# Kernel tuning notes

Hardware: AMD Instinct MI355X
Metric: run time of the kernel (lower is better)

## Reference

```python
import jax, jax.numpy as jnp
import numpy as np

N, E, D_IN, L, H, U = 20000, 320000, 256, 4, 4, 64
HID = H * U  # 256
OUT = 64
LN_EPS = 1e-3  # keras LayerNormalization default epsilon
NEG_SLOPE = 0.2


def layer_norm(x, g, b):
    m = jnp.mean(x, axis=-1, keepdims=True)
    v = jnp.var(x, axis=-1, keepdims=True)
    return (x - m) * jax.lax.rsqrt(v + LN_EPS) * g + b


def gatv2(x, dst, src, Wl, Wr, a):
    # x: [N, HID]; Wl/Wr: [HID, H, U]; a: [H, U]
    zl = jnp.einsum('nd,dhu->nhu', x, Wl)  # target projection
    zr = jnp.einsum('nd,dhu->nhu', x, Wr)  # source projection / messages
    f = jax.nn.leaky_relu(zl[dst] + zr[src], NEG_SLOPE)       # [E, H, U]
    s = jnp.einsum('ehu,hu->eh', f, a)                        # [E, H]
    smax = jax.ops.segment_max(s, dst, num_segments=N)        # [N, H]
    es = jnp.exp(s - smax[dst])
    denom = jax.ops.segment_sum(es, dst, num_segments=N)      # [N, H]
    agg = jax.ops.segment_sum(es[:, :, None] * zr[src], dst, num_segments=N)
    agg = agg / (denom[:, :, None] + 1e-9)                    # [N, H, U]
    return agg.reshape(N, HID) + x  # residual (input dim == H*U)


def setup_inputs() -> dict:
    key = jax.random.key(0)
    ks = jax.random.split(key, 10)
    s_in = 1.0 / np.sqrt(D_IN)
    s_h = 1.0 / np.sqrt(HID)
    return {
        'x': jax.random.normal(ks[0], (N, D_IN), jnp.float32),
        'head_W': jax.random.normal(ks[1], (D_IN, HID), jnp.float32) * s_in,
        'head_b': jnp.zeros((HID,), jnp.float32),
        'ng_g': jnp.ones((L, HID), jnp.float32),
        'ng_b': jnp.zeros((L, HID), jnp.float32),
        'Wl': jax.random.normal(ks[2], (L, HID, H, U), jnp.float32) * s_h,
        'Wr': jax.random.normal(ks[3], (L, HID, H, U), jnp.float32) * s_h,
        'att': jax.random.normal(ks[4], (L, H, U), jnp.float32) * (1.0 / np.sqrt(U)),
        'nd_g': jnp.ones((L, HID), jnp.float32),
        'nd_b': jnp.zeros((L, HID), jnp.float32),
        'dense_W': jax.random.normal(ks[5], (L, HID, 4 * HID), jnp.float32) * s_h,
        'dense_b': jnp.zeros((L, 4 * HID), jnp.float32),
        'tail_W': jax.random.normal(ks[6], (HID, OUT), jnp.float32) * s_h,
        'tail_b': jnp.zeros((OUT,), jnp.float32),
        'edges': jax.random.randint(ks[7], (E, 2), 0, N, jnp.int32),
    }


def reference(x, head_W, head_b, ng_g, ng_b, Wl, Wr, att, nd_g, nd_b,
              dense_W, dense_b, tail_W, tail_b, edges):
    dst, src = edges[:, 0], edges[:, 1]
    h = x @ head_W + head_b  # head_layer
    for l in range(L):
        h = layer_norm(h, ng_g[l], ng_b[l])
        h = gatv2(h, dst, src, Wl[l], Wr[l], att[l])
        xr = layer_norm(h, nd_g[l], nd_b[l])
        # inference: dropout is identity
        d = jax.nn.gelu(xr @ dense_W[l] + dense_b[l], approximate=True)  # [N, 4*HID]
        h = d.reshape(N, 4, HID).sum(axis=1) + xr  # Add(split(.,4)) + residual
    return h @ tail_W + tail_b
```

## Files before the change

### kernel.cpp

```cpp
#include <hip/hip_runtime.h>
#include <cstdint>

#define NN 20000
#define EE 320000
#define DHID 256

typedef short bf16x8 __attribute__((ext_vector_type(8)));
typedef float f32x4 __attribute__((ext_vector_type(4)));


__device__ __forceinline__ float b2f(unsigned short u) {
    union { unsigned int i; float f; } v;
    v.i = ((unsigned int)u) << 16;
    return v.f;
}

__device__ __forceinline__ void b2f2(unsigned int w, float& lo, float& hi) {
    union { unsigned int i; float f; } a, c;
    a.i = w << 16;
    c.i = w & 0xffff0000u;
    lo = a.f;
    hi = c.f;
}

__device__ __forceinline__ unsigned short f2b(float x) {
    union { float f; unsigned int i; } v;
    v.f = x;
    unsigned int r = (v.i + 0x7FFFu + ((v.i >> 16) & 1u)) >> 16;
    return (unsigned short)r;
}

__device__ __forceinline__ float wave_sum(float v) {
#pragma unroll
    for (int m = 1; m < 64; m <<= 1) v += __shfl_xor(v, m);
    return v;
}

#define DPP_ROR_ADD(v, n)                                                                  \
    v += __int_as_float(__builtin_amdgcn_update_dpp(__float_as_int(v), __float_as_int(v),  \
                                                    0x120 + (n), 0xF, 0xF, 0))
__device__ __forceinline__ float quad16_sum(float v) {
    DPP_ROR_ADD(v, 8);
    DPP_ROR_ADD(v, 4);
    DPP_ROR_ADD(v, 2);
    DPP_ROR_ADD(v, 1);
    return v;
}

__device__ __forceinline__ float gelu_f(float x) {
    float z = 0.7978845608028654f * (x + 0.044715f * x * x * x);
    float e = __expf(2.0f * z);
    float t = 1.0f - 2.0f / (e + 1.0f);
    return 0.5f * x * (1.0f + t);
}

__device__ __forceinline__ void gld16(const unsigned short* g, unsigned short* lds) {
    __builtin_amdgcn_global_load_lds((const __attribute__((address_space(1))) unsigned int*)g,
                                     (__attribute__((address_space(3))) unsigned int*)lds, 16, 0, 0);
}


__global__ void hist_kernel(const int* __restrict__ edges, int* __restrict__ counts, int E_) {
    int e = blockIdx.x * 256 + threadIdx.x;
    if (e >= E_) return;
    atomicAdd(&counts[edges[e * 2]], 1);
}

__global__ void pad_counts(const int* __restrict__ counts, int* __restrict__ pc, int n) {
    int i = blockIdx.x * 256 + threadIdx.x;
    if (i < n) pc[i] = (counts[i] + 3) & ~3;
}

__global__ __launch_bounds__(1024) void scan_block(const int* __restrict__ counts,
                                                   int* __restrict__ excl,
                                                   int* __restrict__ bsums, int n) {
    __shared__ int sd[1024];
    int tid = threadIdx.x;
    int i = blockIdx.x * 1024 + tid;
    int c = (i < n) ? counts[i] : 0;
    sd[tid] = c;
    __syncthreads();
#pragma unroll
    for (int off = 1; off < 1024; off <<= 1) {
        int v = (tid >= off) ? sd[tid - off] : 0;
        __syncthreads();
        sd[tid] += v;
        __syncthreads();
    }
    if (i < n) excl[i] = sd[tid] - c;
    if (tid == 1023) bsums[blockIdx.x] = sd[1023];
}

__global__ void scan_tops(int* __restrict__ bsums, int nb) {
    if (threadIdx.x == 0 && blockIdx.x == 0) {
        int run = 0;
        for (int i = 0; i < nb; ++i) { int t = bsums[i]; bsums[i] = run; run += t; }
    }
}

__global__ void scan_fix2(const int* __restrict__ excl, const int* __restrict__ bsums,
                          const int* __restrict__ counts,
                          int* __restrict__ astart, int* __restrict__ aend,
                          int* __restrict__ cursor, int n) {
    int i = blockIdx.x * 256 + threadIdx.x;
    if (i < n) {
        int v = excl[i] + bsums[i >> 10];
        astart[i] = v;
        cursor[i] = v;
        aend[i]   = v + counts[i];
    }
}

__global__ void scatter2(const int* __restrict__ edges, int* __restrict__ cursor,
                         unsigned int* __restrict__ soff, int E_) {
    int e = blockIdx.x * 256 + threadIdx.x;
    if (e >= E_) return;
    int dstn = edges[e * 2];
    int src  = edges[e * 2 + 1];
    int pos = atomicAdd(&cursor[dstn], 1);
    soff[pos] = (unsigned int)src << 10;
}


__global__ __launch_bounds__(256) void transpose_bf16(const float* __restrict__ W,
                                                      unsigned short* __restrict__ Wt,
                                                      int K, int M, size_t lsW, size_t lsT) {
    W  += (size_t)blockIdx.z * lsW;
    Wt += (size_t)blockIdx.z * lsT;
    __shared__ float sm[32][33];
    int m0 = blockIdx.x * 32, k0 = blockIdx.y * 32;
    int tx = threadIdx.x & 31, ty = threadIdx.x >> 5;
#pragma unroll
    for (int i = 0; i < 4; ++i)
        sm[ty + i * 8][tx] = W[(size_t)(k0 + ty + i * 8) * M + m0 + tx];
    __syncthreads();
#pragma unroll
    for (int i = 0; i < 4; ++i)
        Wt[(size_t)(m0 + ty + i * 8) * K + k0 + tx] = f2b(sm[tx][ty + i * 8]);
}

__global__ __launch_bounds__(256) void transpose_perm(const float* __restrict__ W,
                                                      unsigned short* __restrict__ Wt,
                                                      int K, int M, size_t lsW, size_t lsT) {
    W  += (size_t)blockIdx.z * lsW;
    Wt += (size_t)blockIdx.z * lsT;
    __shared__ float sm[32][33];
    int m0 = blockIdx.x * 32, k0 = blockIdx.y * 32;
    int tx = threadIdx.x & 31, ty = threadIdx.x >> 5;
#pragma unroll
    for (int i = 0; i < 4; ++i)
        sm[ty + i * 8][tx] = W[(size_t)(k0 + ty + i * 8) * M + m0 + tx];
    __syncthreads();
#pragma unroll
    for (int i = 0; i < 4; ++i) {
        int mm = m0 + ty + i * 8;
        int c = mm >> 8, j = mm & 255;
        int by = j >> 5, t = j & 31;
        int cc = (by << 7) | ((t >> 4) << 6) | (c << 4) | (t & 15);
        Wt[(size_t)cc * K + k0 + tx] = f2b(sm[tx][ty + i * 8]);
    }
}

__global__ void convert_bf16(const float* __restrict__ in, unsigned short* __restrict__ out, int n4) {
    int i = blockIdx.x * 256 + threadIdx.x;
    if (i >= n4) return;
    float4 v = *(const float4*)(in + (size_t)i * 4);
    ushort4 o;
    o.x = f2b(v.x); o.y = f2b(v.y); o.z = f2b(v.z); o.w = f2b(v.w);
    *(ushort4*)(out + (size_t)i * 4) = o;
}


__global__ __launch_bounds__(256) void ln_kernel(const float* __restrict__ X,
                                                 const float* __restrict__ g,
                                                 const float* __restrict__ b,
                                                 unsigned short* __restrict__ Yb, int nrows) {
    int row = blockIdx.x * 4 + (threadIdx.x >> 6);
    int lane = threadIdx.x & 63;
    if (row >= nrows) return;
    float4 v = *(const float4*)(X + (size_t)row * DHID + lane * 4);
    float sum = wave_sum(v.x + v.y + v.z + v.w);
    float sq  = wave_sum(v.x * v.x + v.y * v.y + v.z * v.z + v.w * v.w);
    float mean = sum * (1.0f / DHID);
    float var  = sq * (1.0f / DHID) - mean * mean;
    float r = rsqrtf(fmaxf(var, 0.0f) + 1e-3f);
    float4 gv = *(const float4*)(g + lane * 4);
    float4 bv = *(const float4*)(b + lane * 4);
    float4 o;
    o.x = (v.x - mean) * r * gv.x + bv.x;
    o.y = (v.y - mean) * r * gv.y + bv.y;
    o.z = (v.z - mean) * r * gv.z + bv.z;
    o.w = (v.w - mean) * r * gv.w + bv.w;
    ushort4 ob;
    ob.x = f2b(o.x); ob.y = f2b(o.y); ob.z = f2b(o.z); ob.w = f2b(o.w);
    *(ushort4*)(Yb + (size_t)row * DHID + lane * 4) = ob;
}

__global__ __launch_bounds__(256) void ln_dense(const unsigned short* __restrict__ d,
                                                const unsigned short* __restrict__ xrb,
                                                const float* __restrict__ g,
                                                const float* __restrict__ b,
                                                unsigned short* __restrict__ Yb, int nrows) {
    int row = blockIdx.x * 4 + (threadIdx.x >> 6);
    int lane = threadIdx.x & 63;
    if (row >= nrows) return;
    ushort4 xu = *(const ushort4*)(xrb + (size_t)row * DHID + lane * 4);
    ushort4 du = *(const ushort4*)(d   + (size_t)row * DHID + lane * 4);
    float4 v;
    v.x = b2f(xu.x) + b2f(du.x);
    v.y = b2f(xu.y) + b2f(du.y);
    v.z = b2f(xu.z) + b2f(du.z);
    v.w = b2f(xu.w) + b2f(du.w);
    float sum = wave_sum(v.x + v.y + v.z + v.w);
    float sq  = wave_sum(v.x * v.x + v.y * v.y + v.z * v.z + v.w * v.w);
    float mean = sum * (1.0f / DHID);
    float var  = sq * (1.0f / DHID) - mean * mean;
    float r = rsqrtf(fmaxf(var, 0.0f) + 1e-3f);
    float4 gv = *(const float4*)(g + lane * 4);
    float4 bv = *(const float4*)(b + lane * 4);
    float4 o;
    o.x = (v.x - mean) * r * gv.x + bv.x;
    o.y = (v.y - mean) * r * gv.y + bv.y;
    o.z = (v.z - mean) * r * gv.z + bv.z;
    o.w = (v.w - mean) * r * gv.w + bv.w;
    ushort4 ob;
    ob.x = f2b(o.x); ob.y = f2b(o.y); ob.z = f2b(o.z); ob.w = f2b(o.w);
    *(ushort4*)(Yb + (size_t)row * DHID + lane * 4) = ob;
}

__global__ __launch_bounds__(256) void combine_final(const unsigned short* __restrict__ d,
                                                     const unsigned short* __restrict__ xrb,
                                                     unsigned short* __restrict__ hb, int nrows) {
    int row = blockIdx.x * 4 + (threadIdx.x >> 6);
    int lane = threadIdx.x & 63;
    if (row >= nrows) return;
    ushort4 xu = *(const ushort4*)(xrb + (size_t)row * DHID + lane * 4);
    ushort4 du = *(const ushort4*)(d   + (size_t)row * DHID + lane * 4);
    ushort4 ob;
    ob.x = f2b(b2f(xu.x) + b2f(du.x));
    ob.y = f2b(b2f(xu.y) + b2f(du.y));
    ob.z = f2b(b2f(xu.z) + b2f(du.z));
    ob.w = f2b(b2f(xu.w) + b2f(du.w));
    *(ushort4*)(hb + (size_t)row * DHID + lane * 4) = ob;
}


#define CS_STRIDE 140
#define CS2_STRIDE 40

template <int EP>
__global__ __launch_bounds__(256, 3) void gemm128(const unsigned short* __restrict__ A,
                                                  const unsigned short* __restrict__ B,
                                                  const float* __restrict__ bias,
                                                  void* __restrict__ Cv, int nrows, int ncols) {
    __shared__ unsigned short smem[128 * CS_STRIDE];
    unsigned short* As = smem;
    unsigned short* Bs = smem + 8192;
    unsigned short* Cs = smem;
    const int bm = blockIdx.x * 128, bn = blockIdx.y * 128;
    if (bm >= nrows) return;
    const int tid  = threadIdx.x;
    const int w    = tid >> 6, lane = tid & 63;
    const int quad = lane >> 4, l16 = lane & 15;
    const int wm = w >> 1, wn = w & 1;

    const int srow = lane & 15;
    const int sg   = lane >> 4;
    int ga0 = min(bm + w * 32 + srow,      nrows - 1);
    int ga1 = min(bm + w * 32 + 16 + srow, nrows - 1);
    int gb0 = min(bn + w * 32 + srow,      ncols - 1);
    int gb1 = min(bn + w * 32 + 16 + srow, ncols - 1);
    const unsigned short* Ap0 = A + (size_t)ga0 * 256 + sg * 8;
    const unsigned short* Ap1 = A + (size_t)ga1 * 256 + sg * 8;
    const unsigned short* Bp0 = B + (size_t)gb0 * 256 + sg * 8;
    const unsigned short* Bp1 = B + (size_t)gb1 * 256 + sg * 8;
    unsigned short* la0 = As + (2 * w) * 1024;
    unsigned short* la1 = As + (2 * w + 1) * 1024;
    unsigned short* lb0 = Bs + (2 * w) * 1024;
    unsigned short* lb1 = Bs + (2 * w + 1) * 1024;

    f32x4 acc[4][4] = {};
    for (int k0 = 0; k0 < 256; k0 += 64) {
        gld16(Ap0 + k0,      la0);
        gld16(Ap0 + k0 + 32, la0 + 512);
        gld16(Ap1 + k0,      la1);
        gld16(Ap1 + k0 + 32, la1 + 512);
        gld16(Bp0 + k0,      lb0);
        gld16(Bp0 + k0 + 32, lb0 + 512);
        gld16(Bp1 + k0,      lb1);
        gld16(Bp1 + k0 + 32, lb1 + 512);
        __syncthreads();
#pragma unroll
        for (int kk = 0; kk < 2; ++kk) {
            bf16x8 a[4], b[4];
#pragma unroll
            for (int mi = 0; mi < 4; ++mi)
                a[mi] = *(const bf16x8*)(As + (wm * 4 + mi) * 1024 + (kk * 4 + quad) * 128 + l16 * 8);
#pragma unroll
            for (int ni = 0; ni < 4; ++ni)
                b[ni] = *(const bf16x8*)(Bs + (wn * 4 + ni) * 1024 + (kk * 4 + quad) * 128 + l16 * 8);
#pragma unroll
            for (int mi = 0; mi < 4; ++mi)
#pragma unroll
                for (int ni = 0; ni < 4; ++ni)
                    acc[mi][ni] = __builtin_amdgcn_mfma_f32_16x16x32_bf16(a[mi], b[ni], acc[mi][ni], 0, 0, 0);
        }
        __syncthreads();
    }

    if (EP == 0) {
#pragma unroll
        for (int ni = 0; ni < 4; ++ni) {
            int col = bn + wn * 64 + ni * 16 + l16;
            if (col >= ncols) continue;
            float bv = bias ? bias[col] : 0.0f;
#pragma unroll
            for (int mi = 0; mi < 4; ++mi) {
#pragma unroll
                for (int r = 0; r < 4; ++r) {
                    int row = bm + wm * 64 + mi * 16 + quad * 4 + r;
                    if (row < nrows) ((float*)Cv)[(size_t)row * ncols + col] = acc[mi][ni][r] + bv;
                }
            }
        }
    } else if (EP == 1) {
#pragma unroll
        for (int ni = 0; ni < 4; ++ni) {
            int lc = wn * 64 + ni * 16 + l16;
#pragma unroll
            for (int mi = 0; mi < 4; ++mi) {
#pragma unroll
                for (int r = 0; r < 4; ++r) {
                    int lr = wm * 64 + mi * 16 + quad * 4 + r;
                    Cs[lr * CS_STRIDE + lc] = f2b(acc[mi][ni][r]);
                }
            }
        }
        __syncthreads();
#pragma unroll
        for (int i = 0; i < 8; ++i) {
            int id = tid + 256 * i;
            int lr = id >> 4;
            int lc = (id & 15) * 8;
            int grow = bm + lr;
            if (grow < nrows) {
                uint4 val = *(const uint4*)(Cs + lr * CS_STRIDE + lc);
                *(uint4*)((unsigned short*)Cv + (size_t)grow * ncols + bn + lc) = val;
            }
        }
    } else {
        unsigned short* Cs2 = smem;
        int jfl = wn * 16 + l16;
        int jf  = (bn >> 2) + jfl;
        float bv0 = bias[jf];
        float bv1 = bias[256 + jf];
        float bv2 = bias[512 + jf];
        float bv3 = bias[768 + jf];
#pragma unroll
        for (int mi = 0; mi < 4; ++mi) {
#pragma unroll
            for (int r = 0; r < 4; ++r) {
                float v = gelu_f(acc[mi][0][r] + bv0) + gelu_f(acc[mi][1][r] + bv1)
                        + gelu_f(acc[mi][2][r] + bv2) + gelu_f(acc[mi][3][r] + bv3);
                int lr = wm * 64 + mi * 16 + quad * 4 + r;
                Cs2[lr * CS2_STRIDE + jfl] = f2b(v);
            }
        }
        __syncthreads();
#pragma unroll
        for (int i = 0; i < 2; ++i) {
            int id = tid + 256 * i;
            int lr = id >> 2;
            int q  = id & 3;
            int grow = bm + lr;
            if (grow < nrows) {
                uint4 val = *(const uint4*)(Cs2 + lr * CS2_STRIDE + q * 8);
                *(uint4*)((unsigned short*)Cv + (size_t)grow * 256 + (bn >> 2) + q * 8) = val;
            }
        }
    }
}


__global__ __launch_bounds__(256) void gat_fused(const unsigned short* __restrict__ zb,
                                                 const float* __restrict__ att,
                                                 const unsigned int* __restrict__ soff,
                                                 const int* __restrict__ astart,
                                                 const int* __restrict__ aend,
                                                 const unsigned short* __restrict__ hnb,
                                                 const float* __restrict__ g,
                                                 const float* __restrict__ b,
                                                 unsigned short* __restrict__ xrb, int nrows) {
    int wid = threadIdx.x >> 6;
    int lane = threadIdx.x & 63;
    int n = blockIdx.x * 4 + wid;
    if (n >= nrows) return;
    int p0  = astart[n];
    int end = aend[n];

    ushort4 zlu = *(const ushort4*)(zb + (size_t)n * 512 + lane * 4);
    float zl0 = b2f(zlu.x), zl1 = b2f(zlu.y), zl2 = b2f(zlu.z), zl3 = b2f(zlu.w);
    float4 a4 = *(const float4*)(att + lane * 4);

    const char* zrb = (const char*)zb + 512;
    const unsigned int loff = (unsigned int)lane * 8u;

    float denom = 0.f;
    float ax = 0.f, ay = 0.f, az = 0.f, aw = 0.f;

    auto edge4 = [&](uint2 u0, uint2 u1, uint2 u2, uint2 u3, int pb) {
        float z00, z01, z02, z03, z10, z11, z12, z13;
        float z20, z21, z22, z23, z30, z31, z32, z33;
        b2f2(u0.x, z00, z01); b2f2(u0.y, z02, z03);
        b2f2(u1.x, z10, z11); b2f2(u1.y, z12, z13);
        b2f2(u2.x, z20, z21); b2f2(u2.y, z22, z23);
        b2f2(u3.x, z30, z31); b2f2(u3.y, z32, z33);

        float v00 = zl0 + z00, v01 = zl1 + z01, v02 = zl2 + z02, v03 = zl3 + z03;
        float v10 = zl0 + z10, v11 = zl1 + z11, v12 = zl2 + z12, v13 = zl3 + z13;
        float v20 = zl0 + z20, v21 = zl1 + z21, v22 = zl2 + z22, v23 = zl3 + z23;
        float v30 = zl0 + z30, v31 = zl1 + z31, v32 = zl2 + z32, v33 = zl3 + z33;
        v00 = fmaxf(v00, 0.2f * v00); v01 = fmaxf(v01, 0.2f * v01);
        v02 = fmaxf(v02, 0.2f * v02); v03 = fmaxf(v03, 0.2f * v03);
        v10 = fmaxf(v10, 0.2f * v10); v11 = fmaxf(v11, 0.2f * v11);
        v12 = fmaxf(v12, 0.2f * v12); v13 = fmaxf(v13, 0.2f * v13);
        v20 = fmaxf(v20, 0.2f * v20); v21 = fmaxf(v21, 0.2f * v21);
        v22 = fmaxf(v22, 0.2f * v22); v23 = fmaxf(v23, 0.2f * v23);
        v30 = fmaxf(v30, 0.2f * v30); v31 = fmaxf(v31, 0.2f * v31);
        v32 = fmaxf(v32, 0.2f * v32); v33 = fmaxf(v33, 0.2f * v33);
        float q0 = a4.x * v00 + a4.y * v01 + a4.z * v02 + a4.w * v03;
        float q1 = a4.x * v10 + a4.y * v11 + a4.z * v12 + a4.w * v13;
        float q2 = a4.x * v20 + a4.y * v21 + a4.z * v22 + a4.w * v23;
        float q3 = a4.x * v30 + a4.y * v31 + a4.z * v32 + a4.w * v33;
        float s0 = quad16_sum(q0);
        float s1 = quad16_sum(q1);
        float s2 = quad16_sum(q2);
        float s3 = quad16_sum(q3);
        float w0 = __expf(s0);
        float w1 = (pb + 1 < end) ? __expf(s1) : 0.0f;
        float w2 = (pb + 2 < end) ? __expf(s2) : 0.0f;
        float w3 = (pb + 3 < end) ? __expf(s3) : 0.0f;
        denom += (w0 + w1) + (w2 + w3);
        ax += (w0 * z00 + w1 * z10) + (w2 * z20 + w3 * z30);
        ay += (w0 * z01 + w1 * z11) + (w2 * z21 + w3 * z31);
        az += (w0 * z02 + w1 * z12) + (w2 * z22 + w3 * z32);
        aw += (w0 * z03 + w1 * z13) + (w2 * z23 + w3 * z33);
    };

    uint4 oA = *(const uint4*)(soff + p0);
    uint2 cA0 = *(const uint2*)(zrb + (oA.x + loff));
    uint2 cA1 = *(const uint2*)(zrb + (oA.y + loff));
    uint2 cA2 = *(const uint2*)(zrb + (oA.z + loff));
    uint2 cA3 = *(const uint2*)(zrb + (oA.w + loff));
    uint4 oB = *(const uint4*)(soff + p0 + 4);
    uint2 cB0 = *(const uint2*)(zrb + (oB.x + loff));
    uint2 cB1 = *(const uint2*)(zrb + (oB.y + loff));
    uint2 cB2 = *(const uint2*)(zrb + (oB.z + loff));
    uint2 cB3 = *(const uint2*)(zrb + (oB.w + loff));

    for (int p = p0; p < end; p += 8) {
        edge4(cA0, cA1, cA2, cA3, p);
        oA = *(const uint4*)(soff + p + 8);
        cA0 = *(const uint2*)(zrb + (oA.x + loff));
        cA1 = *(const uint2*)(zrb + (oA.y + loff));
        cA2 = *(const uint2*)(zrb + (oA.z + loff));
        cA3 = *(const uint2*)(zrb + (oA.w + loff));
        if (p + 4 >= end) break;
        edge4(cB0, cB1, cB2, cB3, p + 4);
        oB = *(const uint4*)(soff + p + 12);
        cB0 = *(const uint2*)(zrb + (oB.x + loff));
        cB1 = *(const uint2*)(zrb + (oB.y + loff));
        cB2 = *(const uint2*)(zrb + (oB.z + loff));
        cB3 = *(const uint2*)(zrb + (oB.w + loff));
    }

    size_t idx = (size_t)n * DHID + lane * 4;
    ushort4 ru = *(const ushort4*)(hnb + idx);
    float inv = 1.0f / (denom + 1e-9f);
    float4 o;
    o.x = ax * inv + b2f(ru.x);
    o.y = ay * inv + b2f(ru.y);
    o.z = az * inv + b2f(ru.z);
    o.w = aw * inv + b2f(ru.w);
    float sum = wave_sum(o.x + o.y + o.z + o.w);
    float sq  = wave_sum(o.x * o.x + o.y * o.y + o.z * o.z + o.w * o.w);
    float mean = sum * (1.0f / DHID);
    float var  = sq * (1.0f / DHID) - mean * mean;
    float rnorm = rsqrtf(fmaxf(var, 0.0f) + 1e-3f);
    float4 gv = *(const float4*)(g + lane * 4);
    float4 bv = *(const float4*)(b + lane * 4);
    float4 y;
    y.x = (o.x - mean) * rnorm * gv.x + bv.x;
    y.y = (o.y - mean) * rnorm * gv.y + bv.y;
    y.z = (o.z - mean) * rnorm * gv.z + bv.z;
    y.w = (o.w - mean) * rnorm * gv.w + bv.w;
    ushort4 ob;
    ob.x = f2b(y.x); ob.y = f2b(y.y); ob.z = f2b(y.z); ob.w = f2b(y.w);
    *(ushort4*)(xrb + idx) = ob;
}


extern "C" void kernel_launch(void* const* d_in, const int* in_sizes, int n_in,
                              void* d_out, int out_size, void* d_ws, size_t ws_size,
                              hipStream_t stream) {
    const float* x       = (const float*)d_in[0];
    const float* head_W  = (const float*)d_in[1];
    const float* head_b  = (const float*)d_in[2];
    const float* ng_g    = (const float*)d_in[3];
    const float* ng_b    = (const float*)d_in[4];
    const float* Wl      = (const float*)d_in[5];
    const float* Wr      = (const float*)d_in[6];
    const float* att     = (const float*)d_in[7];
    const float* nd_g    = (const float*)d_in[8];
    const float* nd_b    = (const float*)d_in[9];
    const float* dense_W = (const float*)d_in[10];
    const float* dense_b = (const float*)d_in[11];
    const float* tail_W  = (const float*)d_in[12];
    const float* tail_b  = (const float*)d_in[13];
    const int*   edges   = (const int*)d_in[14];
    float* out = (float*)d_out;

    const size_t NH = (size_t)NN * DHID;
    const int SOFF_LEN = EE + 4 * NN + 16;
    float* xr = (float*)d_ws;
    float* hn = xr + NH;
    unsigned short* hnb = (unsigned short*)(hn + NH);
    unsigned short* xrb = hnb + NH;
    unsigned short* U   = xrb + NH;
    unsigned short* zb  = U;
    unsigned short* d_buf = U;
    unsigned short* headT  = U + 4 * NH;
    unsigned short* WzT    = headT + 65536;
    unsigned short* denseT = WzT + 524288;
    unsigned short* tailT  = denseT + 1048576;
    int* counts  = (int*)(tailT + 16384);
    int* pcounts = counts + NN;
    int* bsums   = pcounts + NN;
    int* excl    = bsums + 32;
    int* cursor  = excl + NN;
    unsigned int* soff = (unsigned int*)hn;
    int* astart = (int*)(soff + SOFF_LEN);
    int* aendp  = astart + NN;

    hipMemsetAsync(counts, 0, NN * sizeof(int), stream);
    hipMemsetAsync(soff, 0, SOFF_LEN * sizeof(int), stream);
    hist_kernel<<<(EE + 255) / 256, 256, 0, stream>>>(edges, counts, EE);
    pad_counts<<<(NN + 255) / 256, 256, 0, stream>>>(counts, pcounts, NN);
    scan_block<<<(NN + 1023) / 1024, 1024, 0, stream>>>(pcounts, excl, bsums, NN);
    scan_tops<<<1, 64, 0, stream>>>(bsums, (NN + 1023) / 1024);
    scan_fix2<<<(NN + 255) / 256, 256, 0, stream>>>(excl, bsums, counts, astart, aendp, cursor, NN);
    scatter2<<<(EE + 255) / 256, 256, 0, stream>>>(edges, cursor, soff, EE);

    transpose_bf16<<<dim3(8, 8, 1), 256, 0, stream>>>(head_W, headT, 256, 256, 0, 0);
    transpose_bf16<<<dim3(8, 8, 4), 256, 0, stream>>>(Wl, WzT, 256, 256, 65536, 131072);
    transpose_bf16<<<dim3(8, 8, 4), 256, 0, stream>>>(Wr, WzT + 65536, 256, 256, 65536, 131072);
    transpose_perm<<<dim3(32, 8, 4), 256, 0, stream>>>(dense_W, denseT, 256, 1024, 262144, 262144);
    transpose_bf16<<<dim3(2, 8, 1), 256, 0, stream>>>(tail_W, tailT, 256, 64, 0, 0);
    convert_bf16<<<(int)(NH / 4 + 255) / 256, 256, 0, stream>>>(x, hnb, (int)(NH / 4));

    const int GXP = 160;
    gemm128<0><<<dim3(GXP, 2), 256, 0, stream>>>(hnb, headT, head_b, xr, NN, 256);

    for (int l = 0; l < 4; ++l) {
        if (l == 0)
            ln_kernel<<<NN / 4, 256, 0, stream>>>(xr, ng_g, ng_b, hnb, NN);
        else
            ln_dense<<<NN / 4, 256, 0, stream>>>(d_buf, xrb, ng_g + l * 256, ng_b + l * 256, hnb, NN);
        gemm128<1><<<dim3(GXP, 4), 256, 0, stream>>>(hnb, WzT + (size_t)l * 131072, nullptr, zb, NN, 512);
        gat_fused<<<(NN + 3) / 4, 256, 0, stream>>>(zb, att + l * 256, soff, astart, aendp, hnb,
                                                    nd_g + l * 256, nd_b + l * 256, xrb, NN);
        gemm128<3><<<dim3(GXP, 8), 256, 0, stream>>>(xrb, denseT + (size_t)l * 262144,
                                                     dense_b + l * 1024, d_buf, NN, 1024);
    }
    combine_final<<<NN / 4, 256, 0, stream>>>(d_buf, xrb, hnb, NN);
    gemm128<0><<<dim3(GXP, 1), 256, 0, stream>>>(hnb, tailT, tail_b, out, NN, 64);
}
```

Baseline: 541.7 us.

## Sort nodes by degree bucket for GAT load balance and simplify GELU

```diff
diff --git a/kernel.cpp b/kernel.cpp
--- a/kernel.cpp
+++ b/kernel.cpp
@@ -48,10 +48,11 @@
 }
 
 __device__ __forceinline__ float gelu_f(float x) {
-    float z = 0.7978845608028654f * (x + 0.044715f * x * x * x);
-    float e = __expf(2.0f * z);
-    float t = 1.0f - 2.0f / (e + 1.0f);
-    return 0.5f * x * (1.0f + t);
+    float x2 = x * x;
+    float p  = fmaf(0.044715f, x2, 1.0f);
+    float e  = __expf(x * p * 1.5957691216f);
+    float r  = 1.0f / (e + 1.0f);
+    return x - x * r;
 }
 
 __device__ __forceinline__ void gld16(const unsigned short* g, unsigned short* lds) {
@@ -119,6 +120,28 @@
     int src  = edges[e * 2 + 1];
     int pos = atomicAdd(&cursor[dstn], 1);
     soff[pos] = (unsigned int)src << 10;
+}
+
+
+__global__ void deg_hist(const int* __restrict__ counts, int* __restrict__ dh, int n) {
+    int i = blockIdx.x * 256 + threadIdx.x;
+    if (i < n) atomicAdd(&dh[min((counts[i] + 3) >> 2, 63)], 1);
+}
+
+__global__ void deg_scan(int* __restrict__ dh) {
+    if (threadIdx.x == 0 && blockIdx.x == 0) {
+        int run = 0;
+        for (int i = 0; i < 64; ++i) { int t = dh[i]; dh[i] = run; run += t; }
+    }
+}
+
+__global__ void deg_scatter(const int* __restrict__ counts, int* __restrict__ dh,
+                            int* __restrict__ norder, int n) {
+    int i = blockIdx.x * 256 + threadIdx.x;
+    if (i < n) {
+        int pos = atomicAdd(&dh[min((counts[i] + 3) >> 2, 63)], 1);
+        norder[pos] = i;
+    }
 }
 
 
@@ -387,14 +410,16 @@
                                                  const unsigned int* __restrict__ soff,
                                                  const int* __restrict__ astart,
                                                  const int* __restrict__ aend,
+                                                 const int* __restrict__ norder,
                                                  const unsigned short* __restrict__ hnb,
                                                  const float* __restrict__ g,
                                                  const float* __restrict__ b,
                                                  unsigned short* __restrict__ xrb, int nrows) {
     int wid = threadIdx.x >> 6;
     int lane = threadIdx.x & 63;
-    int n = blockIdx.x * 4 + wid;
-    if (n >= nrows) return;
+    int n0 = blockIdx.x * 4 + wid;
+    if (n0 >= nrows) return;
+    int n   = norder[n0];
     int p0  = astart[n];
     int end = aend[n];
 
@@ -541,11 +566,17 @@
     unsigned int* soff = (unsigned int*)hn;
     int* astart = (int*)(soff + SOFF_LEN);
     int* aendp  = astart + NN;
+    int* norder = aendp + NN;
+    int* dh     = norder + NN;
 
     hipMemsetAsync(counts, 0, NN * sizeof(int), stream);
+    hipMemsetAsync(dh, 0, 64 * sizeof(int), stream);
     hipMemsetAsync(soff, 0, SOFF_LEN * sizeof(int), stream);
     hist_kernel<<<(EE + 255) / 256, 256, 0, stream>>>(edges, counts, EE);
     pad_counts<<<(NN + 255) / 256, 256, 0, stream>>>(counts, pcounts, NN);
+    deg_hist<<<(NN + 255) / 256, 256, 0, stream>>>(counts, dh, NN);
+    deg_scan<<<1, 64, 0, stream>>>(dh);
+    deg_scatter<<<(NN + 255) / 256, 256, 0, stream>>>(counts, dh, norder, NN);
     scan_block<<<(NN + 1023) / 1024, 1024, 0, stream>>>(pcounts, excl, bsums, NN);
     scan_tops<<<1, 64, 0, stream>>>(bsums, (NN + 1023) / 1024);
     scan_fix2<<<(NN + 255) / 256, 256, 0, stream>>>(excl, bsums, counts, astart, aendp, cursor, NN);
@@ -567,7 +598,7 @@
         else
             ln_dense<<<NN / 4, 256, 0, stream>>>(d_buf, xrb, ng_g + l * 256, ng_b + l * 256, hnb, NN);
         gemm128<1><<<dim3(GXP, 4), 256, 0, stream>>>(hnb, WzT + (size_t)l * 131072, nullptr, zb, NN, 512);
-        gat_fused<<<(NN + 3) / 4, 256, 0, stream>>>(zb, att + l * 256, soff, astart, aendp, hnb,
+        gat_fused<<<(NN + 3) / 4, 256, 0, stream>>>(zb, att + l * 256, soff, astart, aendp, norder, hnb,
                                                     nd_g + l * 256, nd_b + l * 256, xrb, NN);
         gemm128<3><<<dim3(GXP, 8), 256, 0, stream>>>(xrb, denseT + (size_t)l * 262144,
                                                      dense_b + l * 1024, d_buf, NN, 1024);
```

New measurement: 768.4 us. 41.8% more time.
